# Performance work log

Hardware: AMD Instinct MI355X
Metric: run time of the kernel (lower is better)

## Reference

```python
import jax, jax.numpy as jnp
import numpy as np

N_NODES = 50000
N_EDGES = 800000
HID = 256
HEADS = 4
HEAD_C = HID // HEADS  # 64
IN_CH = 16
OUT_CH = 4
NEG_SLOPE = 0.2  # PyG GATConv default LeakyReLU slope
LN_EPS = 1e-5


def setup_inputs() -> dict:
    key = jax.random.key(0)
    ks = jax.random.split(key, 12)
    s = 0.05
    return {
        "x": jax.random.normal(ks[0], (N_NODES, IN_CH), dtype=jnp.float32),
        "edge_index": jax.random.randint(ks[1], (2, N_EDGES), 0, N_NODES, dtype=jnp.int64),
        "w_in": jax.random.normal(ks[2], (IN_CH, HID), dtype=jnp.float32) * s,
        "b_in": jnp.zeros((HID,), dtype=jnp.float32),
        "w_gat": jax.random.normal(ks[3], (4, HID, HID), dtype=jnp.float32) * s,
        "att_src": jax.random.normal(ks[4], (4, HEADS, HEAD_C), dtype=jnp.float32) * s,
        "att_dst": jax.random.normal(ks[5], (4, HEADS, HEAD_C), dtype=jnp.float32) * s,
        "b_gat": jnp.zeros((4, HID), dtype=jnp.float32),
        "ln_scale": jnp.ones((4, HID), dtype=jnp.float32),
        "ln_bias": jnp.zeros((4, HID), dtype=jnp.float32),
        "w_out": jax.random.normal(ks[6], (HID, OUT_CH), dtype=jnp.float32) * s,
        "b_out": jnp.zeros((OUT_CH,), dtype=jnp.float32),
    }


def _gat_layer(x, src, dst, W, a_src, a_dst, bias, g, beta):
    """One GATConv(concat, heads=4) + LayerNorm + ELU. x:[N,HID]."""
    n = x.shape[0]
    h = (x @ W).reshape(n, HEADS, HEAD_C)                 # [N,H,C]
    a_s = jnp.einsum("nhc,hc->nh", h, a_src)              # [N,H]
    a_d = jnp.einsum("nhc,hc->nh", h, a_dst)              # [N,H]
    logits = jax.nn.leaky_relu(a_s[src] + a_d[dst], NEG_SLOPE)  # [E,H]
    # segment softmax over destination neighborhoods (self-loops ensure non-empty)
    m = jax.ops.segment_max(logits, dst, num_segments=n)
    e = jnp.exp(logits - m[dst])
    denom = jax.ops.segment_sum(e, dst, num_segments=n)
    alpha = e / (denom[dst] + 1e-16)                      # [E,H]
    msg = alpha[:, :, None] * h[src]                      # [E,H,C]
    out = jax.ops.segment_sum(msg, dst, num_segments=n).reshape(n, HID) + bias
    mu = out.mean(-1, keepdims=True)
    var = out.var(-1, keepdims=True)
    out = (out - mu) * jax.lax.rsqrt(var + LN_EPS) * g + beta
    return jax.nn.elu(out)


def reference(x, edge_index, w_in, b_in, w_gat, att_src, att_dst, b_gat,
              ln_scale, ln_bias, w_out, b_out):
    n = x.shape[0]
    # PyG GATConv adds self-loops by default
    loops = jnp.arange(n, dtype=edge_index.dtype)
    ei = jnp.concatenate([edge_index, jnp.stack([loops, loops])], axis=1)
    src, dst = ei[0], ei[1]

    x = x @ w_in + b_in                                   # input_proj
    h = x
    for l in (0, 1):
        h = _gat_layer(h, src, dst, w_gat[l], att_src[l], att_dst[l],
                       b_gat[l], ln_scale[l], ln_bias[l])
    x = x + h
    h = x
    for l in (2, 3):
        h = _gat_layer(h, src, dst, w_gat[l], att_src[l], att_dst[l],
                       b_gat[l], ln_scale[l], ln_bias[l])
    x = x + h
    return x @ w_out + b_out
```

## Files before the change

### kernel.cpp

```cpp
#include <hip/hip_runtime.h>
#include <math.h>

#define NN 50000
#define E0 800000
#define ET 850000
#define HID 256
#define INCH 16

typedef _Float16 h8 __attribute__((ext_vector_type(8)));
typedef float f32x4 __attribute__((ext_vector_type(4)));

__device__ __forceinline__ void load_lds16(const void* g, void* l) {
    __builtin_amdgcn_global_load_lds(
        (const __attribute__((address_space(1))) unsigned int*)g,
        (__attribute__((address_space(3))) unsigned int*)l, 16, 0, 0);
}

__global__ void hist_kernel(const int* __restrict__ ei, int* __restrict__ counts) {
    int e = blockIdx.x * blockDim.x + threadIdx.x;
    if (e >= ET) return;
    int d = (e < E0) ? ei[E0 + e] : (e - E0);
    atomicAdd(&counts[d], 1);
}

__global__ void scan1_kernel(const int* __restrict__ counts, int* __restrict__ incl,
                             int* __restrict__ bsums, int n) {
    __shared__ int sh[256];
    int t = threadIdx.x, i = blockIdx.x * 256 + t;
    int v = (i < n) ? counts[i] : 0;
    sh[t] = v;
    __syncthreads();
    for (int off = 1; off < 256; off <<= 1) {
        int add = (t >= off) ? sh[t - off] : 0;
        __syncthreads();
        sh[t] += add;
        __syncthreads();
    }
    if (i < n) incl[i] = sh[t];
    if (t == 255) bsums[blockIdx.x] = sh[255];
}

__global__ void scan2_kernel(int* __restrict__ bsums, int nb) {
    __shared__ int sh[256];
    int t = threadIdx.x;
    int v = (t < nb) ? bsums[t] : 0;
    sh[t] = v;
    __syncthreads();
    for (int off = 1; off < 256; off <<= 1) {
        int add = (t >= off) ? sh[t - off] : 0;
        __syncthreads();
        sh[t] += add;
        __syncthreads();
    }
    if (t < nb) bsums[t] = sh[t];
}

__global__ void scan3_kernel(const int* __restrict__ incl, const int* __restrict__ bsums,
                             int* __restrict__ offsets, int n) {
    int i = blockIdx.x * 256 + threadIdx.x;
    if (i < n) {
        int pre = (blockIdx.x > 0) ? bsums[blockIdx.x - 1] : 0;
        offsets[i + 1] = incl[i] + pre;
    }
    if (i == 0) offsets[0] = 0;
}

__global__ void scatter_kernel(const int* __restrict__ ei, const int* __restrict__ offsets,
                               int* __restrict__ cursor, int* __restrict__ csr) {
    int e = blockIdx.x * blockDim.x + threadIdx.x;
    if (e >= ET) return;
    int s, d;
    if (e < E0) { s = ei[e]; d = ei[E0 + e]; }
    else        { s = d = e - E0; }
    int pos = atomicAdd(&cursor[d], 1);
    csr[offsets[d] + pos] = s;
}

__global__ __launch_bounds__(256) void wt_kernel(const float* __restrict__ w,
                                                 _Float16* __restrict__ wt) {
    int k = blockIdx.x, l = blockIdx.y, n = threadIdx.x;
    float v = w[((size_t)l * 256 + k) * 256 + n];
    wt[((size_t)l * 256 + n) * 256 + k] = (_Float16)v;
}

__global__ __launch_bounds__(256) void input_proj_kernel(
    const float* __restrict__ x, const float* __restrict__ w,
    const float* __restrict__ b, _Float16* __restrict__ outh) {
    int n = blockIdx.x, j = threadIdx.x;
    __shared__ float xs[INCH];
    if (j < INCH) xs[j] = x[n * INCH + j];
    __syncthreads();
    float acc = b[j];
#pragma unroll
    for (int k = 0; k < INCH; k++) acc += xs[k] * w[k * HID + j];
    outh[n * HID + j] = (_Float16)acc;
}

__global__ __launch_bounds__(256) void gemm_fused_kernel(
    const _Float16* __restrict__ A, const _Float16* __restrict__ BT,
    _Float16* __restrict__ H, const float* __restrict__ att_s,
    const float* __restrict__ att_d, float* __restrict__ AS, float* __restrict__ AD,
    int N) {
    __shared__ _Float16 As[128 * 32];
    __shared__ _Float16 Bs[128 * 32];
    int t = threadIdx.x;
    int wv = t >> 6, lane = t & 63;
    int rb = blockIdx.x * 128, cb = blockIdx.y * 128;
    int wr = (wv >> 1) * 64, wc = (wv & 1) * 64;
    int lm = lane & 15, lq = lane >> 4;
    f32x4 acc[4][4] = {};

    int rch = lane >> 2;
    int q = lane & 3;

    for (int k0 = 0; k0 < 256; k0 += 32) {
#pragma unroll
        for (int c = 0; c < 2; ++c) {
            int r = wv * 32 + c * 16 + rch;
            int g = q ^ (r & 3);
            int ra = rb + r; if (ra >= N) ra = N - 1;
            load_lds16(A + (size_t)ra * 256 + k0 + g * 8,
                       (char*)As + wv * 2048 + c * 1024);
            load_lds16(BT + (size_t)(cb + r) * 256 + k0 + g * 8,
                       (char*)Bs + wv * 2048 + c * 1024);
        }
        __syncthreads();
        h8 af[4], bfr[4];
#pragma unroll
        for (int i = 0; i < 4; ++i) {
            int row = wr + i * 16 + lm;
            af[i] = *(const h8*)((const char*)As + row * 64 + ((lq ^ (row & 3)) * 16));
        }
#pragma unroll
        for (int j = 0; j < 4; ++j) {
            int row = wc + j * 16 + lm;
            bfr[j] = *(const h8*)((const char*)Bs + row * 64 + ((lq ^ (row & 3)) * 16));
        }
#pragma unroll
        for (int i = 0; i < 4; ++i)
#pragma unroll
            for (int j = 0; j < 4; ++j)
                acc[i][j] = __builtin_amdgcn_mfma_f32_16x16x32_f16(af[i], bfr[j], acc[i][j], 0, 0, 0);
        __syncthreads();
    }

    int head = (cb + wc) >> 6;
    float sa[4], sd[4];
#pragma unroll
    for (int j = 0; j < 4; ++j) {
        sa[j] = att_s[head * 64 + j * 16 + lm];
        sd[j] = att_d[head * 64 + j * 16 + lm];
    }
#pragma unroll
    for (int i = 0; i < 4; ++i)
#pragma unroll
        for (int rr = 0; rr < 4; ++rr) {
            float vs = acc[i][0][rr] * sa[0] + acc[i][1][rr] * sa[1]
                     + acc[i][2][rr] * sa[2] + acc[i][3][rr] * sa[3];
            float vd = acc[i][0][rr] * sd[0] + acc[i][1][rr] * sd[1]
                     + acc[i][2][rr] * sd[2] + acc[i][3][rr] * sd[3];
#pragma unroll
            for (int o = 1; o <= 8; o <<= 1) {
                vs += __shfl_xor(vs, o, 64);
                vd += __shfl_xor(vd, o, 64);
            }
            int row = rb + wr + i * 16 + lq * 4 + rr;
            if (lm == 0 && row < N) {
                AS[row * 4 + head] = vs;
                AD[row * 4 + head] = vd;
            }
        }

#pragma unroll
    for (int i = 0; i < 4; ++i)
#pragma unroll
        for (int j = 0; j < 4; ++j) {
            int col = cb + wc + j * 16 + lm;
#pragma unroll
            for (int rr = 0; rr < 4; ++rr) {
                int row = rb + wr + i * 16 + lq * 4 + rr;
                if (row < N) H[(size_t)row * 256 + col] = (_Float16)acc[i][j][rr];
            }
        }
}

__global__ __launch_bounds__(256) void agg_kernel(
    const _Float16* __restrict__ H, const float4* __restrict__ AS,
    const float4* __restrict__ AD,
    const int* __restrict__ offs, const int* __restrict__ csr,
    const float* __restrict__ bias, const float* __restrict__ g, const float* __restrict__ beta,
    const _Float16* __restrict__ res, _Float16* __restrict__ outh) {
    int t = threadIdx.x;
    int l32 = t & 31;
    int n = blockIdx.x * 8 + (t >> 5);
    int start = offs[n], end = offs[n + 1];
    float4 adv = AD[n];
    int head = l32 >> 3;
    int c0 = l32 * 8;
    float advh = (head == 0) ? adv.x : (head == 1) ? adv.y : (head == 2) ? adv.z : adv.w;

    float acc[8] = {};
    float acc_e = 0.f;
#pragma unroll 2
    for (int i = start; i < end; ++i) {
        int s = csr[i];
        const float* as = (const float*)&AS[s];
        float v = as[head] + advh;
        v = (v >= 0.f) ? v : 0.2f * v;
        float e = __expf(v);
        acc_e += e;
        h8 hv = *(const h8*)(H + (size_t)s * 256 + c0);
#pragma unroll
        for (int k = 0; k < 8; ++k) acc[k] += e * (float)hv[k];
    }
    float dinv = 1.f / (acc_e + 1e-16f);

    float val[8];
#pragma unroll
    for (int k = 0; k < 8; k += 4) {
        float4 bb = *(const float4*)(bias + c0 + k);
        val[k]     = acc[k]     * dinv + bb.x;
        val[k + 1] = acc[k + 1] * dinv + bb.y;
        val[k + 2] = acc[k + 2] * dinv + bb.z;
        val[k + 3] = acc[k + 3] * dinv + bb.w;
    }

    float s1 = 0.f, s2 = 0.f;
#pragma unroll
    for (int k = 0; k < 8; ++k) { s1 += val[k]; s2 += val[k] * val[k]; }
#pragma unroll
    for (int o = 16; o >= 1; o >>= 1) {
        s1 += __shfl_xor(s1, o, 64);
        s2 += __shfl_xor(s2, o, 64);
    }
    float mu = s1 * (1.f / 256.f);
    float var = s2 * (1.f / 256.f) - mu * mu;
    float rs = rsqrtf(var + 1e-5f);

    float y[8];
#pragma unroll
    for (int k = 0; k < 8; k += 4) {
        float4 g4 = *(const float4*)(g + c0 + k);
        float4 b4 = *(const float4*)(beta + c0 + k);
        y[k]     = (val[k]     - mu) * rs * g4.x + b4.x;
        y[k + 1] = (val[k + 1] - mu) * rs * g4.y + b4.y;
        y[k + 2] = (val[k + 2] - mu) * rs * g4.z + b4.z;
        y[k + 3] = (val[k + 3] - mu) * rs * g4.w + b4.w;
    }
#pragma unroll
    for (int k = 0; k < 8; ++k) y[k] = (y[k] > 0.f) ? y[k] : (__expf(y[k]) - 1.f);
    if (res) {
        h8 r0 = *(const h8*)(res + (size_t)n * 256 + c0);
#pragma unroll
        for (int k = 0; k < 8; ++k) y[k] += (float)r0[k];
    }
    h8 o0;
#pragma unroll
    for (int k = 0; k < 8; ++k) o0[k] = (_Float16)y[k];
    *(h8*)(outh + (size_t)n * 256 + c0) = o0;
}

__global__ __launch_bounds__(256) void out_proj_kernel(
    const _Float16* __restrict__ x, const float* __restrict__ w,
    const float* __restrict__ b, float* __restrict__ out, int n) {
    int tid = blockIdx.x * blockDim.x + threadIdx.x;
    int node = tid >> 6, lane = tid & 63;
    if (node >= n) return;
    const _Float16* xp = x + (size_t)node * HID + lane * 4;
    float x0 = (float)xp[0], x1 = (float)xp[1], x2 = (float)xp[2], x3 = (float)xp[3];
    const float4* wr = (const float4*)w;
    float4 w0 = wr[lane * 4 + 0];
    float4 w1 = wr[lane * 4 + 1];
    float4 w2 = wr[lane * 4 + 2];
    float4 w3 = wr[lane * 4 + 3];
    float o0 = x0 * w0.x + x1 * w1.x + x2 * w2.x + x3 * w3.x;
    float o1 = x0 * w0.y + x1 * w1.y + x2 * w2.y + x3 * w3.y;
    float o2 = x0 * w0.z + x1 * w1.z + x2 * w2.z + x3 * w3.z;
    float o3 = x0 * w0.w + x1 * w1.w + x2 * w2.w + x3 * w3.w;
#pragma unroll
    for (int o = 32; o >= 1; o >>= 1) {
        o0 += __shfl_down(o0, o, 64);
        o1 += __shfl_down(o1, o, 64);
        o2 += __shfl_down(o2, o, 64);
        o3 += __shfl_down(o3, o, 64);
    }
    if (lane == 0) {
        out[node * 4 + 0] = o0 + b[0];
        out[node * 4 + 1] = o1 + b[1];
        out[node * 4 + 2] = o2 + b[2];
        out[node * 4 + 3] = o3 + b[3];
    }
}

extern "C" void kernel_launch(void* const* d_in, const int* in_sizes, int n_in,
                              void* d_out, int out_size, void* d_ws, size_t ws_size,
                              hipStream_t stream) {
    const float* x       = (const float*)d_in[0];
    const int*   ei      = (const int*)  d_in[1];
    const float* w_in    = (const float*)d_in[2];
    const float* b_in    = (const float*)d_in[3];
    const float* w_gat   = (const float*)d_in[4];
    const float* att_src = (const float*)d_in[5];
    const float* att_dst = (const float*)d_in[6];
    const float* b_gat   = (const float*)d_in[7];
    const float* ln_g    = (const float*)d_in[8];
    const float* ln_b    = (const float*)d_in[9];
    const float* w_out   = (const float*)d_in[10];
    const float* b_out   = (const float*)d_in[11];
    float* out = (float*)d_out;

    char* ws = (char*)d_ws;
    size_t off = 0;
    auto alloc = [&](size_t bytes) {
        void* p = ws + off;
        off += (bytes + 255) & ~(size_t)255;
        return p;
    };
    _Float16*  Ph   = (_Float16*)alloc((size_t)NN * HID * 2);
    _Float16*  Ch   = (_Float16*)alloc((size_t)NN * HID * 2);
    _Float16*  Gh   = (_Float16*)alloc((size_t)NN * HID * 2);
    _Float16*  H    = (_Float16*)alloc((size_t)NN * HID * 2);
    _Float16*  WT   = (_Float16*)alloc((size_t)4 * HID * HID * 2);
    float*     ASAD = (float*)alloc((size_t)NN * 8 * 4);
    int* counts  = (int*)alloc((size_t)NN * 4);
    int* cursor  = (int*)alloc((size_t)NN * 4);
    int* incl    = (int*)alloc((size_t)NN * 4);
    int* bsums   = (int*)alloc(256 * 4);
    int* offsets = (int*)alloc((size_t)(NN + 1) * 4);
    int* csr     = (int*)alloc((size_t)ET * 4);

    float* AS = ASAD;
    float* AD = ASAD + (size_t)NN * 4;

    const int NB_SCAN = (NN + 255) / 256;
    const int NB_EDGE = (ET + 255) / 256;
    const dim3 GEMM_GRID((NN + 127) / 128, 2);
    const int NB_AGG = NN / 8;

    hipMemsetAsync(counts, 0, 2 * (((size_t)NN * 4 + 255) & ~(size_t)255), stream);
    hist_kernel<<<NB_EDGE, 256, 0, stream>>>(ei, counts);
    scan1_kernel<<<NB_SCAN, 256, 0, stream>>>(counts, incl, bsums, NN);
    scan2_kernel<<<1, 256, 0, stream>>>(bsums, NB_SCAN);
    scan3_kernel<<<NB_SCAN, 256, 0, stream>>>(incl, bsums, offsets, NN);
    scatter_kernel<<<NB_EDGE, 256, 0, stream>>>(ei, offsets, cursor, csr);

    wt_kernel<<<dim3(256, 4), 256, 0, stream>>>(w_gat, WT);
    input_proj_kernel<<<NN, 256, 0, stream>>>(x, w_in, b_in, Ph);

    auto run_layer = [&](const _Float16* inh, int l, const _Float16* res, _Float16* outh) {
        gemm_fused_kernel<<<GEMM_GRID, 256, 0, stream>>>(
            inh, WT + (size_t)l * HID * HID, H,
            att_src + l * 256, att_dst + l * 256, AS, AD, NN);
        agg_kernel<<<NB_AGG, 256, 0, stream>>>(
            H, (const float4*)AS, (const float4*)AD, offsets, csr,
            b_gat + l * 256, ln_g + l * 256, ln_b + l * 256, res, outh);
    };

    run_layer(Ph, 0, nullptr, Gh);
    run_layer(Gh, 1, Ph,      Ch);
    run_layer(Ch, 2, nullptr, Gh);
    run_layer(Gh, 3, Ch,      Ph);

    out_proj_kernel<<<(NN * 64 + 255) / 256, 256, 0, stream>>>(Ph, w_out, b_out, out, NN);
}
```

Measured before the change: 602.8 us.

## Widen GEMM tile to full 256 columns with 512-thread blocks

The GAT projection GEMM now gives each block a 128x256 output tile using 8 waves, instead of splitting columns across two blocks. This means each A row tile is loaded once rather than twice, and the grid becomes one-dimensional. LDS use per block rises, and the block count halves, which may lower occupancy. The aggregation edge loop unroll is also raised from 2 to 4 to expose more memory-level parallelism.

```diff
diff --git a/kernel.cpp b/kernel.cpp
--- a/kernel.cpp
+++ b/kernel.cpp
@@ -96,35 +96,36 @@
     outh[n * HID + j] = (_Float16)acc;
 }
 
-__global__ __launch_bounds__(256) void gemm_fused_kernel(
+__global__ __launch_bounds__(512) void gemm_fused_kernel(
     const _Float16* __restrict__ A, const _Float16* __restrict__ BT,
     _Float16* __restrict__ H, const float* __restrict__ att_s,
     const float* __restrict__ att_d, float* __restrict__ AS, float* __restrict__ AD,
     int N) {
     __shared__ _Float16 As[128 * 32];
-    __shared__ _Float16 Bs[128 * 32];
+    __shared__ _Float16 Bs[256 * 32];
     int t = threadIdx.x;
     int wv = t >> 6, lane = t & 63;
-    int rb = blockIdx.x * 128, cb = blockIdx.y * 128;
-    int wr = (wv >> 1) * 64, wc = (wv & 1) * 64;
+    int rb = blockIdx.x * 128;
+    int wr = (wv >> 2) * 64, wc = (wv & 3) * 64;
     int lm = lane & 15, lq = lane >> 4;
     f32x4 acc[4][4] = {};
 
-    int rch = lane >> 2;
+    int rl = lane >> 2;
     int q = lane & 3;
 
     for (int k0 = 0; k0 < 256; k0 += 32) {
-#pragma unroll
-        for (int c = 0; c < 2; ++c) {
-            int r = wv * 32 + c * 16 + rch;
-            int g = q ^ (r & 3);
-            int ra = rb + r; if (ra >= N) ra = N - 1;
-            load_lds16(A + (size_t)ra * 256 + k0 + g * 8,
-                       (char*)As + wv * 2048 + c * 1024);
-            load_lds16(BT + (size_t)(cb + r) * 256 + k0 + g * 8,
-                       (char*)Bs + wv * 2048 + c * 1024);
-        }
-        __syncthreads();
+        int rA = wv * 16 + rl;
+        int gA = q ^ (rA & 3);
+        int raA = rb + rA; if (raA >= N) raA = N - 1;
+        load_lds16(A + (size_t)raA * 256 + k0 + gA * 8, (char*)As + wv * 1024);
+        int rB0 = wv * 32 + rl;
+        int gB0 = q ^ (rB0 & 3);
+        load_lds16(BT + (size_t)rB0 * 256 + k0 + gB0 * 8, (char*)Bs + wv * 2048);
+        int rB1 = rB0 + 16;
+        int gB1 = q ^ (rB1 & 3);
+        load_lds16(BT + (size_t)rB1 * 256 + k0 + gB1 * 8, (char*)Bs + wv * 2048 + 1024);
+        __syncthreads();
+
         h8 af[4], bfr[4];
 #pragma unroll
         for (int i = 0; i < 4; ++i) {
@@ -144,7 +145,7 @@
         __syncthreads();
     }
 
-    int head = (cb + wc) >> 6;
+    int head = wv & 3;
     float sa[4], sd[4];
 #pragma unroll
     for (int j = 0; j < 4; ++j) {
@@ -175,7 +176,7 @@
     for (int i = 0; i < 4; ++i)
 #pragma unroll
         for (int j = 0; j < 4; ++j) {
-            int col = cb + wc + j * 16 + lm;
+            int col = wc + j * 16 + lm;
 #pragma unroll
             for (int rr = 0; rr < 4; ++rr) {
                 int row = rb + wr + i * 16 + lq * 4 + rr;
@@ -201,7 +202,7 @@
 
     float acc[8] = {};
     float acc_e = 0.f;
-#pragma unroll 2
+#pragma unroll 4
     for (int i = start; i < end; ++i) {
         int s = csr[i];
         const float* as = (const float*)&AS[s];
@@ -334,7 +335,7 @@
 
     const int NB_SCAN = (NN + 255) / 256;
     const int NB_EDGE = (ET + 255) / 256;
-    const dim3 GEMM_GRID((NN + 127) / 128, 2);
+    const int NB_GEMM = (NN + 127) / 128;
     const int NB_AGG = NN / 8;
 
     hipMemsetAsync(counts, 0, 2 * (((size_t)NN * 4 + 255) & ~(size_t)255), stream);
@@ -348,7 +349,7 @@
     input_proj_kernel<<<NN, 256, 0, stream>>>(x, w_in, b_in, Ph);
 
     auto run_layer = [&](const _Float16* inh, int l, const _Float16* res, _Float16* outh) {
-        gemm_fused_kernel<<<GEMM_GRID, 256, 0, stream>>>(
+        gemm_fused_kernel<<<NB_GEMM, 512, 0, stream>>>(
             inh, WT + (size_t)l * HID * HID, H,
             att_src + l * 256, att_dst + l * 256, AS, AD, NN);
         agg_kernel<<<NB_AGG, 256, 0, stream>>>(
```

Result: no change. 604.7 us (+0.3%).
